# Kernel tuning notes

Measured on AMD Instinct MI355X. Metric: run time of the kernel, lower is better.

## Reference

```python
import jax, jax.numpy as jnp
import numpy as np

DN = ('NHWC', 'HWIO', 'NHWC')

def conv_same(x, w):
    return jax.lax.conv_general_dilated(x, w, (1, 1), 'SAME', dimension_numbers=DN)

def hard_sigmoid(x):
    # Keras ConvLSTM2D default recurrent_activation='hard_sigmoid'
    return jnp.clip(0.2 * x + 0.5, 0.0, 1.0)

def setup_inputs() -> dict:
    key = jax.random.key(0)
    ks = jax.random.split(key, 20)
    B, T, H, W, C = 4, 10, 144, 256, 3
    F = 64  # ConvLSTM filters
    def w(k, shape, fan_in):
        return jax.random.normal(k, shape, jnp.float32) * (1.0 / np.sqrt(fan_in))
    inp = {}
    inp['inputs'] = jax.random.normal(ks[0], (B, T, H, W, C), jnp.float32)
    # ConvLSTM2D: input kernel, recurrent kernel, bias (gate order i, f, c, o)
    inp['Wx'] = w(ks[1], (5, 5, C, 4 * F), 5 * 5 * C)
    inp['Wh'] = w(ks[2], (5, 5, F, 4 * F), 5 * 5 * F)
    inp['b_lstm'] = jnp.zeros((4 * F,), jnp.float32)
    # BatchNorm (inference mode: moving stats)
    inp['gamma'] = jnp.ones((F,), jnp.float32)
    inp['beta'] = jnp.zeros((F,), jnp.float32)
    inp['mov_mean'] = jax.random.normal(ks[3], (F,), jnp.float32) * 0.1
    inp['mov_var'] = jax.random.uniform(ks[4], (F,), jnp.float32, 0.5, 1.5)
    # Conv2D stack
    inp['W1'] = w(ks[5], (9, 9, 64, 16), 9 * 9 * 64); inp['b1'] = jnp.zeros((16,), jnp.float32)
    inp['W2'] = w(ks[6], (5, 5, 16, 32), 5 * 5 * 16); inp['b2'] = jnp.zeros((32,), jnp.float32)
    inp['W3'] = w(ks[7], (3, 3, 32, 64), 3 * 3 * 32); inp['b3'] = jnp.zeros((64,), jnp.float32)
    inp['W4'] = w(ks[8], (3, 3, 64, 64), 3 * 3 * 64); inp['b4'] = jnp.zeros((64,), jnp.float32)
    inp['W5'] = w(ks[9], (3, 3, 64, 3), 3 * 3 * 64); inp['b5'] = jnp.zeros((3,), jnp.float32)
    return inp

def conv_lstm(inputs, Wx, Wh, b_lstm):
    B, T, H, W, _ = inputs.shape
    F = Wh.shape[2]
    xs = jnp.transpose(inputs, (1, 0, 2, 3, 4))  # [T,B,H,W,C]

    def step(carry, x_t):
        h, c = carry
        z = conv_same(x_t, Wx) + b_lstm + conv_same(h, Wh)  # [B,H,W,4F]
        zi, zf, zc, zo = jnp.split(z, 4, axis=-1)
        i = hard_sigmoid(zi)
        f = hard_sigmoid(zf)
        o = hard_sigmoid(zo)
        c_new = f * c + i * jnp.tanh(zc)
        h_new = o * jnp.tanh(c_new)
        return (h_new, c_new), None

    h0 = jnp.zeros((B, H, W, F), inputs.dtype)
    c0 = jnp.zeros((B, H, W, F), inputs.dtype)
    (h, _), _ = jax.lax.scan(step, (h0, c0), xs)
    return h  # return_sequences=False -> last hidden state

def reference(inputs, Wx, Wh, b_lstm, gamma, beta, mov_mean, mov_var,
              W1, b1, W2, b2, W3, b3, W4, b4, W5, b5):
    X = conv_lstm(inputs, Wx, Wh, b_lstm)
    # BatchNorm inference, eps=1e-3 (Keras default)
    X = (X - mov_mean) * jax.lax.rsqrt(mov_var + 1e-3) * gamma + beta
    X = jax.nn.relu(conv_same(X, W1) + b1)
    X = jax.nn.relu(conv_same(X, W2) + b2)
    X = jax.nn.relu(conv_same(X, W3) + b3)
    X = jax.nn.relu(conv_same(X, W4) + b4)
    X = jax.nn.sigmoid(conv_same(X, W5) + b5)
    return X
```

## Files before the change

### kernel.cpp

```cpp
#include <hip/hip_runtime.h>
#include <math.h>

#define B_ 4
#define T_ 10
#define H_ 144
#define W_ 256
#define F_ 64

typedef __attribute__((ext_vector_type(8))) __bf16 bf16x8;
typedef __attribute__((ext_vector_type(4))) float f32x4;

static __device__ __forceinline__ float hs_(float x) {
    return fminf(fmaxf(fmaf(x, 0.2f, 0.5f), 0.f), 1.f);
}
static __device__ __forceinline__ unsigned short f2bf(float f) {
    unsigned u = __builtin_bit_cast(unsigned, f);
    u += 0x7fff + ((u >> 16) & 1);
    return (unsigned short)(u >> 16);
}
static __device__ __forceinline__ float bf2f(unsigned short s) {
    unsigned u = ((unsigned)s) << 16;
    return __builtin_bit_cast(float, u);
}

__global__ void repack_wh_mfma(const float* __restrict__ w, unsigned short* __restrict__ o) {
    int idx = blockIdx.x * 256 + threadIdx.x;
    if (idx >= 25 * 2 * 4 * 4 * 64) return;
    int l = idx & 63;
    int wf = (idx >> 6) & 3;
    int g = (idx >> 8) & 3;
    int ch = (idx >> 10) & 1;
    int tap = idx >> 11;
    int n = g * 64 + wf * 16 + (l & 15);
    unsigned short* dst = o + (size_t)idx * 8;
#pragma unroll
    for (int j = 0; j < 8; ++j) {
        int c = ch * 32 + (l >> 4) * 8 + j;
        dst[j] = f2bf(w[((size_t)(tap * 64 + c)) * 256 + n]);
    }
}

__global__ void repack_wx_mfma(const float* __restrict__ w, unsigned short* __restrict__ o) {
    int idx = blockIdx.x * 256 + threadIdx.x;
    if (idx >= 5 * 4 * 4 * 64) return;
    int l = idx & 63;
    int wf = (idx >> 6) & 3;
    int g = (idx >> 8) & 3;
    int ky = idx >> 10;
    int n = g * 64 + wf * 16 + (l & 15);
    unsigned short* dst = o + (size_t)idx * 8;
#pragma unroll
    for (int j = 0; j < 8; ++j) {
        int k = (l >> 4) * 8 + j;
        unsigned short v = 0;
        if (k < 15) {
            int kx = k / 3, c = k - kx * 3;
            v = f2bf(w[((size_t)((ky * 5 + kx) * 3 + c)) * 256 + n]);
        }
        dst[j] = v;
    }
}

__global__ void repack_conv(const float* __restrict__ w, unsigned short* __restrict__ o,
                            int taps, int cin, int cout) {
    int NF = cout >> 4;
    int total = taps * 2 * NF * 64;
    int idx = blockIdx.x * 256 + threadIdx.x;
    if (idx >= total) return;
    int l = idx & 63;
    int nf = (idx >> 6) % NF;
    int ch = ((idx >> 6) / NF) & 1;
    int tap = (idx >> 6) / NF / 2;
    int n = nf * 16 + (l & 15);
    unsigned short* dst = o + (size_t)idx * 8;
#pragma unroll
    for (int j = 0; j < 8; ++j) {
        int c = ch * 32 + (l >> 4) * 8 + j;
        dst[j] = (c < cin) ? f2bf(w[((size_t)(tap * cin + c)) * cout + n]) : (unsigned short)0;
    }
}

#define MT 64
__global__ __launch_bounds__(256, 3) void lstm_mfma(
    const float* __restrict__ x,
    const unsigned short* __restrict__ wxr,
    const unsigned short* __restrict__ whr,
    const float* __restrict__ bias,
    const unsigned short* __restrict__ h_prev,
    unsigned short* __restrict__ h_out,
    float* __restrict__ c_io,
    int t, int first)
{
    __shared__ char sh[5 * 68 * 128];
    __shared__ unsigned short sxr[5 * 72 * 4];

    const int b = blockIdx.z, y = blockIdx.y, x0 = blockIdx.x * MT;
    const int tid = threadIdx.x;
    const int w = tid >> 6, l = tid & 63;
    const int m0 = l & 15, kq = l >> 4;

    int dj[8];
#pragma unroll
    for (int j = 0; j < 8; ++j) {
        int k = kq * 8 + j;
        int kx = k / 3, c = k - kx * 3;
        dj[j] = (k < 15) ? kx * 4 + c : 3;
    }

    for (int e = tid; e < 5 * 68; e += 256) {
        int ky = e / 68, px = e - ky * 68;
        sxr[(ky * 72 + px) * 4 + 3] = 0;
    }
    for (int e = tid; e < 5 * 68 * 3; e += 256) {
        int ky = e / 204;
        int rem = e - ky * 204;
        int px = rem / 3, c = rem - px * 3;
        int yg = y + ky - 2, xg = x0 + px - 2;
        float v = 0.f;
        if (yg >= 0 && yg < H_ && (unsigned)xg < W_)
            v = x[(((size_t)((b * T_ + t) * H_ + yg)) * W_ + xg) * 3 + c];
        sxr[(ky * 72 + px) * 4 + c] = f2bf(v);
    }
    if (!first) {
        for (int e = tid; e < 5 * 68 * 8; e += 256) {
            int ky = e / (68 * 8);
            int rem = e - ky * 68 * 8;
            int px = rem >> 3, cg = rem & 7;
            int yg = y + ky - 2, xg = x0 + px - 2;
            uint4 v = make_uint4(0, 0, 0, 0);
            if (yg >= 0 && yg < H_ && (unsigned)xg < W_)
                v = *(const uint4*)(h_prev + ((((size_t)(b * H_ + yg)) * W_ + xg) << 6) + cg * 8);
            int slot = ((cg & 3) << 1) | (cg >> 2);
            int off = ((ky * 68 + px) * 128 + slot * 16) ^ ((px & 7) << 4);
            *(uint4*)(sh + off) = v;
        }
    }
    __syncthreads();

    f32x4 acc[4][4];
#pragma unroll
    for (int rf = 0; rf < 4; ++rf)
#pragma unroll
        for (int g = 0; g < 4; ++g) acc[rf][g] = (f32x4){0.f, 0.f, 0.f, 0.f};

    for (int ky = 0; ky < 5; ++ky) {
        bf16x8 a[4], bb[4];
#pragma unroll
        for (int rf = 0; rf < 4; ++rf) {
            int base = (ky * 72 + rf * 16 + m0) * 4;
            union { bf16x8 v; unsigned short u[8]; } tt;
#pragma unroll
            for (int j = 0; j < 8; ++j) tt.u[j] = sxr[base + dj[j]];
            a[rf] = tt.v;
        }
#pragma unroll
        for (int g = 0; g < 4; ++g)
            bb[g] = *(const bf16x8*)(wxr + ((size_t)((ky * 16 + g * 4 + w) * 64 + l)) * 8);
#pragma unroll
        for (int rf = 0; rf < 4; ++rf)
#pragma unroll
            for (int g = 0; g < 4; ++g)
                acc[rf][g] = __builtin_amdgcn_mfma_f32_16x16x32_bf16(a[rf], bb[g], acc[rf][g], 0, 0, 0);
    }

    if (!first) {
        int V[5][2];
#pragma unroll
        for (int kx = 0; kx < 5; ++kx) {
            int T = ((m0 + kx) & 7) << 4;
#pragma unroll
            for (int ch = 0; ch < 2; ++ch)
                V[kx][ch] = (m0 * 128 + kq * 32 + ch * 16) ^ T;
        }
        const char* shb = sh;
        const unsigned short* wb = whr + (size_t)w * 512 + (size_t)l * 8;
#pragma unroll
        for (int ky = 0; ky < 5; ++ky)
#pragma unroll
        for (int kx = 0; kx < 5; ++kx)
#pragma unroll
        for (int ch = 0; ch < 2; ++ch) {
            const int s = (ky * 5 + kx) * 2 + ch;
            bf16x8 a[4], bb[4];
#pragma unroll
            for (int g = 0; g < 4; ++g)
                bb[g] = *(const bf16x8*)(wb + s * 8192 + g * 2048);
#pragma unroll
            for (int rf = 0; rf < 4; ++rf)
                a[rf] = *(const bf16x8*)(shb + (V[kx][ch] + (ky * 8704 + kx * 128 + rf * 2048)));
#pragma unroll
            for (int rf = 0; rf < 4; ++rf)
#pragma unroll
                for (int g = 0; g < 4; ++g)
                    acc[rf][g] = __builtin_amdgcn_mfma_f32_16x16x32_bf16(a[rf], bb[g], acc[rf][g], 0, 0, 0);
        }
    }

    const int f = (w << 4) + m0;
    const float bi0 = bias[f], bi1 = bias[64 + f], bi2 = bias[128 + f], bi3 = bias[192 + f];
#pragma unroll
    for (int rf = 0; rf < 4; ++rf) {
#pragma unroll
        for (int r = 0; r < 4; ++r) {
            int px = x0 + rf * 16 + kq * 4 + r;
            size_t idx = ((((size_t)(b * H_ + y)) * W_ + px) << 6) + f;
            float zi = acc[rf][0][r] + bi0;
            float zf = acc[rf][1][r] + bi1;
            float zc = acc[rf][2][r] + bi2;
            float zo = acc[rf][3][r] + bi3;
            float cp = first ? 0.f : c_io[idx];
            float cn = hs_(zf) * cp + hs_(zi) * tanhf(zc);
            float hn = hs_(zo) * tanhf(cn);
            c_io[idx] = cn;
            h_out[idx] = f2bf(hn);
        }
    }
}

__global__ void bn_k(const unsigned short* __restrict__ in, unsigned short* __restrict__ out,
                     const float* __restrict__ gamma, const float* __restrict__ beta,
                     const float* __restrict__ mean, const float* __restrict__ var, int n) {
    for (int i = blockIdx.x * blockDim.x + threadIdx.x; i < n; i += gridDim.x * blockDim.x) {
        int c = i & 63;
        float s = rsqrtf(var[c] + 1e-3f) * gamma[c];
        out[i] = f2bf((bf2f(in[i]) - mean[c]) * s + beta[c]);
    }
}

template <int KH, int KW, int CIN, int COUT, int KYB>
__global__ __launch_bounds__(256) void conv_mfma(
    const unsigned short* __restrict__ in, const unsigned short* __restrict__ wr,
    const float* __restrict__ bias, unsigned short* __restrict__ out)
{
    constexpr int TC = 64 + KW - 1;
    constexpr int PADX = KW / 2, PADY = KH / 2;
    constexpr int NF = COUT / 16;
    constexpr int CHN = (CIN + 31) / 32;
    constexpr int NKG = KH / KYB;
    __shared__ char sh[KYB * TC * 128];

    const int b = blockIdx.z, y = blockIdx.y, x0 = blockIdx.x * 64;
    const int tid = threadIdx.x;
    const int w = tid >> 6, l = tid & 63;
    const int m0 = l & 15, kq = l >> 4;

    f32x4 acc[NF];
#pragma unroll
    for (int nf = 0; nf < NF; ++nf) acc[nf] = (f32x4){0.f, 0.f, 0.f, 0.f};

    for (int kg = 0; kg < NKG; ++kg) {
        __syncthreads();
        for (int e = tid; e < KYB * TC * 8; e += 256) {
            int kyl = e / (TC * 8);
            int rem = e - kyl * TC * 8;
            int px = rem >> 3, cg = rem & 7;
            int ky = kg * KYB + kyl;
            int yg = y + ky - PADY, xg = x0 + px - PADX;
            int c0 = cg * 8;
            uint4 v = make_uint4(0, 0, 0, 0);
            if (yg >= 0 && yg < H_ && (unsigned)xg < W_ && c0 < CIN)
                v = *(const uint4*)(in + ((size_t)((b * H_ + yg) * W_) + xg) * CIN + c0);
            int off = ((kyl * TC + px) * 128 + cg * 16) ^ ((px & 7) << 4);
            *(uint4*)(sh + off) = v;
        }
        __syncthreads();

        for (int kyl = 0; kyl < KYB; ++kyl) {
            int ky = kg * KYB + kyl;
#pragma unroll
            for (int kx = 0; kx < KW; ++kx) {
#pragma unroll
                for (int ch = 0; ch < CHN; ++ch) {
                    int px = w * 16 + m0 + kx;
                    int off = ((kyl * TC + px) * 128 + ch * 64 + kq * 16) ^ ((px & 7) << 4);
                    bf16x8 a = *(const bf16x8*)(sh + off);
                    int tap = ky * KW + kx;
                    const unsigned short* wp = wr + ((size_t)(((tap * 2 + ch) * NF) * 64 + l)) * 8;
#pragma unroll
                    for (int nf = 0; nf < NF; ++nf) {
                        bf16x8 bb = *(const bf16x8*)(wp + nf * 512);
                        acc[nf] = __builtin_amdgcn_mfma_f32_16x16x32_bf16(a, bb, acc[nf], 0, 0, 0);
                    }
                }
            }
        }
    }

#pragma unroll
    for (int nf = 0; nf < NF; ++nf) {
        int cout = nf * 16 + m0;
        float bv = bias[cout];
#pragma unroll
        for (int r = 0; r < 4; ++r) {
            int px = x0 + w * 16 + kq * 4 + r;
            float v = fmaxf(acc[nf][r] + bv, 0.f);
            out[((size_t)((b * H_ + y) * W_) + px) * COUT + cout] = f2bf(v);
        }
    }
}

__global__ __launch_bounds__(256) void conv5_k(
    const unsigned short* __restrict__ in, const float* __restrict__ wgt,
    const float* __restrict__ bias, float* __restrict__ out)
{
    constexpr int CC = 16;
    __shared__ float s[3][W_ + 2][CC + 1];
    const int b = blockIdx.z, y = blockIdx.y;
    const int tid = threadIdx.x;

    float acc[3] = {0.f, 0.f, 0.f};
    for (int c0 = 0; c0 < 64; c0 += CC) {
        __syncthreads();
        for (int e = tid; e < 3 * (W_ + 2) * CC; e += 256) {
            int r = e / ((W_ + 2) * CC);
            int rem = e % ((W_ + 2) * CC);
            int cc = rem / CC, ch = rem % CC;
            int yg = y + r - 1, xg = cc - 1;
            float v = 0.f;
            if (yg >= 0 && yg < H_ && xg >= 0 && xg < W_)
                v = bf2f(in[((b * H_ + yg) * W_ + xg) * 64 + c0 + ch]);
            s[r][cc][ch] = v;
        }
        __syncthreads();
        for (int ky = 0; ky < 3; ++ky) {
#pragma unroll
            for (int kx = 0; kx < 3; ++kx) {
                for (int c = 0; c < CC; ++c) {
                    const float* wp = &wgt[((ky * 3 + kx) * 64 + c0 + c) * 3];
                    float v = s[ky][tid + kx][c];
                    acc[0] = fmaf(v, wp[0], acc[0]);
                    acc[1] = fmaf(v, wp[1], acc[1]);
                    acc[2] = fmaf(v, wp[2], acc[2]);
                }
            }
        }
    }
#pragma unroll
    for (int j = 0; j < 3; ++j) {
        float v = acc[j] + bias[j];
        v = 1.f / (1.f + expf(-v));
        out[((b * H_ + y) * W_ + tid) * 3 + j] = v;
    }
}

extern "C" void kernel_launch(void* const* d_in, const int* in_sizes, int n_in,
                              void* d_out, int out_size, void* d_ws, size_t ws_size,
                              hipStream_t stream) {
    const float* x     = (const float*)d_in[0];
    const float* Wx    = (const float*)d_in[1];
    const float* Wh    = (const float*)d_in[2];
    const float* bl    = (const float*)d_in[3];
    const float* gamma = (const float*)d_in[4];
    const float* beta  = (const float*)d_in[5];
    const float* mmean = (const float*)d_in[6];
    const float* mvar  = (const float*)d_in[7];
    const float* W1 = (const float*)d_in[8];
    const float* b1 = (const float*)d_in[9];
    const float* W2 = (const float*)d_in[10];
    const float* b2 = (const float*)d_in[11];
    const float* W3 = (const float*)d_in[12];
    const float* b3 = (const float*)d_in[13];
    const float* W4 = (const float*)d_in[14];
    const float* b4 = (const float*)d_in[15];
    const float* W5 = (const float*)d_in[16];
    const float* b5 = (const float*)d_in[17];
    float* out = (float*)d_out;

    const size_t NHWF = (size_t)B_ * H_ * W_ * 64;
    char* p = (char*)d_ws;
    float* c_buf = (float*)p;                 p += NHWF * 4;
    unsigned short* hA = (unsigned short*)p;  p += NHWF * 2;
    unsigned short* hB = (unsigned short*)p;  p += NHWF * 2;
    unsigned short* whr = (unsigned short*)p; p += (size_t)25 * 2 * 16 * 64 * 8 * 2;
    unsigned short* wxr = (unsigned short*)p; p += (size_t)5 * 16 * 64 * 8 * 2;
    unsigned short* w1r = (unsigned short*)p; p += (size_t)81 * 2 * 1 * 512 * 2;
    unsigned short* w2r = (unsigned short*)p; p += (size_t)25 * 2 * 2 * 512 * 2;
    unsigned short* w3r = (unsigned short*)p; p += (size_t)9 * 2 * 4 * 512 * 2;
    unsigned short* w4r = (unsigned short*)p; p += (size_t)9 * 2 * 4 * 512 * 2;

    repack_wh_mfma<<<(25 * 2 * 4 * 4 * 64 + 255) / 256, 256, 0, stream>>>(Wh, whr);
    repack_wx_mfma<<<(5 * 4 * 4 * 64 + 255) / 256, 256, 0, stream>>>(Wx, wxr);
    repack_conv<<<(81 * 2 * 1 * 64 + 255) / 256, 256, 0, stream>>>(W1, w1r, 81, 64, 16);
    repack_conv<<<(25 * 2 * 2 * 64 + 255) / 256, 256, 0, stream>>>(W2, w2r, 25, 16, 32);
    repack_conv<<<(9 * 2 * 4 * 64 + 255) / 256, 256, 0, stream>>>(W3, w3r, 9, 32, 64);
    repack_conv<<<(9 * 2 * 4 * 64 + 255) / 256, 256, 0, stream>>>(W4, w4r, 9, 64, 64);

    dim3 lgrid(W_ / MT, H_, B_);
    for (int t = 0; t < T_; ++t) {
        const unsigned short* hp = (t & 1) ? hA : hB;
        unsigned short* ho = (t & 1) ? hB : hA;
        lstm_mfma<<<lgrid, 256, 0, stream>>>(x, wxr, whr, bl, hp, ho, c_buf, t, t == 0 ? 1 : 0);
    }

    unsigned short* bnb = hA;
    bn_k<<<2048, 256, 0, stream>>>(hB, bnb, gamma, beta, mmean, mvar, (int)NHWF);

    unsigned short* o1 = (unsigned short*)c_buf;
    unsigned short* o2 = o1 + NHWF / 4;
    unsigned short* o3 = hB;
    unsigned short* o4 = hA;

    dim3 cgrid(W_ / 64, H_, B_);
    conv_mfma<9, 9, 64, 16, 3><<<cgrid, 256, 0, stream>>>(bnb, w1r, b1, o1);
    conv_mfma<5, 5, 16, 32, 5><<<cgrid, 256, 0, stream>>>(o1, w2r, b2, o2);
    conv_mfma<3, 3, 32, 64, 3><<<cgrid, 256, 0, stream>>>(o2, w3r, b3, o3);
    conv_mfma<3, 3, 64, 64, 3><<<cgrid, 256, 0, stream>>>(o3, w4r, b4, o4);
    conv5_k<<<dim3(1, H_, B_), 256, 0, stream>>>(o4, W5, b5, out);
}
```

Before: 1.517 ms.

## Compute two output rows per LSTM block to reuse weight fragments

Each LSTM block now covers two image rows instead of one. It stages a 6-row halo of x and h in shared memory and keeps two sets of accumulators, so each loaded weight fragment feeds MFMAs for both rows. This halves the weight traffic per output and reduces halo redundancy. The cost is double the accumulator registers (occupancy hint lowered from 3 to 2 blocks), more LDS, and half as many blocks. The shared-memory channel slot layout and its swizzle addressing are also changed.

```diff
diff --git a/kernel.cpp b/kernel.cpp
--- a/kernel.cpp
+++ b/kernel.cpp
@@ -81,7 +81,7 @@
 }
 
 #define MT 64
-__global__ __launch_bounds__(256, 3) void lstm_mfma(
+__global__ __launch_bounds__(256, 2) void lstm_mfma(
     const float* __restrict__ x,
     const unsigned short* __restrict__ wxr,
     const unsigned short* __restrict__ whr,
@@ -91,10 +91,10 @@
     float* __restrict__ c_io,
     int t, int first)
 {
-    __shared__ char sh[5 * 68 * 128];
-    __shared__ unsigned short sxr[5 * 72 * 4];
-
-    const int b = blockIdx.z, y = blockIdx.y, x0 = blockIdx.x * MT;
+    __shared__ char sh[6 * 68 * 128];
+    __shared__ unsigned short sxr[6 * 72 * 4];
+
+    const int b = blockIdx.z, y0 = blockIdx.y * 2, x0 = blockIdx.x * MT;
     const int tid = threadIdx.x;
     const int w = tid >> 6, l = tid & 63;
     const int m0 = l & 15, kq = l >> 4;
@@ -107,60 +107,66 @@
         dj[j] = (k < 15) ? kx * 4 + c : 3;
     }
 
-    for (int e = tid; e < 5 * 68; e += 256) {
-        int ky = e / 68, px = e - ky * 68;
-        sxr[(ky * 72 + px) * 4 + 3] = 0;
-    }
-    for (int e = tid; e < 5 * 68 * 3; e += 256) {
-        int ky = e / 204;
-        int rem = e - ky * 204;
+    for (int e = tid; e < 6 * 68; e += 256) {
+        int r = e / 68, px = e - r * 68;
+        sxr[(r * 72 + px) * 4 + 3] = 0;
+    }
+    for (int e = tid; e < 6 * 68 * 3; e += 256) {
+        int r = e / 204;
+        int rem = e - r * 204;
         int px = rem / 3, c = rem - px * 3;
-        int yg = y + ky - 2, xg = x0 + px - 2;
+        int yg = y0 + r - 2, xg = x0 + px - 2;
         float v = 0.f;
         if (yg >= 0 && yg < H_ && (unsigned)xg < W_)
             v = x[(((size_t)((b * T_ + t) * H_ + yg)) * W_ + xg) * 3 + c];
-        sxr[(ky * 72 + px) * 4 + c] = f2bf(v);
+        sxr[(r * 72 + px) * 4 + c] = f2bf(v);
     }
     if (!first) {
-        for (int e = tid; e < 5 * 68 * 8; e += 256) {
-            int ky = e / (68 * 8);
-            int rem = e - ky * 68 * 8;
+        for (int e = tid; e < 6 * 68 * 8; e += 256) {
+            int r = e / (68 * 8);
+            int rem = e - r * 68 * 8;
             int px = rem >> 3, cg = rem & 7;
-            int yg = y + ky - 2, xg = x0 + px - 2;
+            int yg = y0 + r - 2, xg = x0 + px - 2;
             uint4 v = make_uint4(0, 0, 0, 0);
             if (yg >= 0 && yg < H_ && (unsigned)xg < W_)
                 v = *(const uint4*)(h_prev + ((((size_t)(b * H_ + yg)) * W_ + xg) << 6) + cg * 8);
-            int slot = ((cg & 3) << 1) | (cg >> 2);
-            int off = ((ky * 68 + px) * 128 + slot * 16) ^ ((px & 7) << 4);
+            int off = ((r * 68 + px) * 128 + cg * 16) ^ ((px & 7) << 4);
             *(uint4*)(sh + off) = v;
         }
     }
     __syncthreads();
 
-    f32x4 acc[4][4];
-#pragma unroll
-    for (int rf = 0; rf < 4; ++rf)
-#pragma unroll
-        for (int g = 0; g < 4; ++g) acc[rf][g] = (f32x4){0.f, 0.f, 0.f, 0.f};
-
+    f32x4 acc[2][4][4];
+#pragma unroll
+    for (int r = 0; r < 2; ++r)
+#pragma unroll
+        for (int rf = 0; rf < 4; ++rf)
+#pragma unroll
+            for (int g = 0; g < 4; ++g) acc[r][rf][g] = (f32x4){0.f, 0.f, 0.f, 0.f};
+
+#pragma unroll
     for (int ky = 0; ky < 5; ++ky) {
-        bf16x8 a[4], bb[4];
-#pragma unroll
-        for (int rf = 0; rf < 4; ++rf) {
-            int base = (ky * 72 + rf * 16 + m0) * 4;
-            union { bf16x8 v; unsigned short u[8]; } tt;
-#pragma unroll
-            for (int j = 0; j < 8; ++j) tt.u[j] = sxr[base + dj[j]];
-            a[rf] = tt.v;
-        }
+        bf16x8 bb[4];
 #pragma unroll
         for (int g = 0; g < 4; ++g)
             bb[g] = *(const bf16x8*)(wxr + ((size_t)((ky * 16 + g * 4 + w) * 64 + l)) * 8);
 #pragma unroll
-        for (int rf = 0; rf < 4; ++rf)
-#pragma unroll
-            for (int g = 0; g < 4; ++g)
-                acc[rf][g] = __builtin_amdgcn_mfma_f32_16x16x32_bf16(a[rf], bb[g], acc[rf][g], 0, 0, 0);
+        for (int r = 0; r < 2; ++r) {
+            bf16x8 a[4];
+#pragma unroll
+            for (int rf = 0; rf < 4; ++rf) {
+                int base = ((ky + r) * 72 + rf * 16 + m0) * 4;
+                union { bf16x8 v; unsigned short u[8]; } tt;
+#pragma unroll
+                for (int j = 0; j < 8; ++j) tt.u[j] = sxr[base + dj[j]];
+                a[rf] = tt.v;
+            }
+#pragma unroll
+            for (int rf = 0; rf < 4; ++rf)
+#pragma unroll
+                for (int g = 0; g < 4; ++g)
+                    acc[r][rf][g] = __builtin_amdgcn_mfma_f32_16x16x32_bf16(a[rf], bb[g], acc[r][rf][g], 0, 0, 0);
+        }
     }
 
     if (!first) {
@@ -170,7 +176,7 @@
             int T = ((m0 + kx) & 7) << 4;
 #pragma unroll
             for (int ch = 0; ch < 2; ++ch)
-                V[kx][ch] = (m0 * 128 + kq * 32 + ch * 16) ^ T;
+                V[kx][ch] = ((m0 + kx) * 128 + ch * 64 + kq * 16) ^ T;
         }
         const char* shb = sh;
         const unsigned short* wb = whr + (size_t)w * 512 + (size_t)l * 8;
@@ -181,38 +187,45 @@
 #pragma unroll
         for (int ch = 0; ch < 2; ++ch) {
             const int s = (ky * 5 + kx) * 2 + ch;
-            bf16x8 a[4], bb[4];
+            bf16x8 bb[4];
 #pragma unroll
             for (int g = 0; g < 4; ++g)
                 bb[g] = *(const bf16x8*)(wb + s * 8192 + g * 2048);
 #pragma unroll
-            for (int rf = 0; rf < 4; ++rf)
-                a[rf] = *(const bf16x8*)(shb + (V[kx][ch] + (ky * 8704 + kx * 128 + rf * 2048)));
-#pragma unroll
-            for (int rf = 0; rf < 4; ++rf)
-#pragma unroll
-                for (int g = 0; g < 4; ++g)
-                    acc[rf][g] = __builtin_amdgcn_mfma_f32_16x16x32_bf16(a[rf], bb[g], acc[rf][g], 0, 0, 0);
+            for (int r = 0; r < 2; ++r) {
+                bf16x8 a[4];
+#pragma unroll
+                for (int rf = 0; rf < 4; ++rf)
+                    a[rf] = *(const bf16x8*)(shb + (V[kx][ch] + ((ky + r) * 8704 + rf * 2048)));
+#pragma unroll
+                for (int rf = 0; rf < 4; ++rf)
+#pragma unroll
+                    for (int g = 0; g < 4; ++g)
+                        acc[r][rf][g] = __builtin_amdgcn_mfma_f32_16x16x32_bf16(a[rf], bb[g], acc[r][rf][g], 0, 0, 0);
+            }
         }
     }
 
     const int f = (w << 4) + m0;
     const float bi0 = bias[f], bi1 = bias[64 + f], bi2 = bias[128 + f], bi3 = bias[192 + f];
 #pragma unroll
-    for (int rf = 0; rf < 4; ++rf) {
-#pragma unroll
-        for (int r = 0; r < 4; ++r) {
-            int px = x0 + rf * 16 + kq * 4 + r;
-            size_t idx = ((((size_t)(b * H_ + y)) * W_ + px) << 6) + f;
-            float zi = acc[rf][0][r] + bi0;
-            float zf = acc[rf][1][r] + bi1;
-            float zc = acc[rf][2][r] + bi2;
-            float zo = acc[rf][3][r] + bi3;
-            float cp = first ? 0.f : c_io[idx];
-            float cn = hs_(zf) * cp + hs_(zi) * tanhf(zc);
-            float hn = hs_(zo) * tanhf(cn);
-            c_io[idx] = cn;
-            h_out[idx] = f2bf(hn);
+    for (int r = 0; r < 2; ++r) {
+#pragma unroll
+        for (int rf = 0; rf < 4; ++rf) {
+#pragma unroll
+            for (int j = 0; j < 4; ++j) {
+                int px = x0 + rf * 16 + kq * 4 + j;
+                size_t idx = ((((size_t)(b * H_ + y0 + r)) * W_ + px) << 6) + f;
+                float zi = acc[r][rf][0][j] + bi0;
+                float zf = acc[r][rf][1][j] + bi1;
+                float zc = acc[r][rf][2][j] + bi2;
+                float zo = acc[r][rf][3][j] + bi3;
+                float cp = first ? 0.f : c_io[idx];
+                float cn = hs_(zf) * cp + hs_(zi) * tanhf(zc);
+                float hn = hs_(zo) * tanhf(cn);
+                c_io[idx] = cn;
+                h_out[idx] = f2bf(hn);
+            }
         }
     }
 }
@@ -385,7 +398,7 @@
     repack_conv<<<(9 * 2 * 4 * 64 + 255) / 256, 256, 0, stream>>>(W3, w3r, 9, 32, 64);
     repack_conv<<<(9 * 2 * 4 * 64 + 255) / 256, 256, 0, stream>>>(W4, w4r, 9, 64, 64);
 
-    dim3 lgrid(W_ / MT, H_, B_);
+    dim3 lgrid(W_ / MT, H_ / 2, B_);
     for (int t = 0; t < T_; ++t) {
         const unsigned short* hp = (t & 1) ? hA : hB;
         unsigned short* ho = (t & 1) ? hB : hA;
```

Measured after the change: 2.416 ms. 59.3% more time.

## Stage recurrent weights through double-buffered LDS via async global_load_lds

Applied to the files above, without the earlier changes.

Recurrent-kernel weight tiles are now staged through a double-buffered 32KB LDS area using global_load_lds, with the next tap's tile prefetched while the current tap's MFMAs run. Before, each wave read them straight from global memory. The hidden-state LDS layout and swizzle are also changed to a plain channel-group order with a new address formula. The changes add a __syncthreads per tap (50 per block) and extra LDS use, so launch bounds drop occupancy from 3 to 2 blocks per CU.

```diff
diff --git a/kernel.cpp b/kernel.cpp
--- a/kernel.cpp
+++ b/kernel.cpp
@@ -21,6 +21,11 @@
 static __device__ __forceinline__ float bf2f(unsigned short s) {
     unsigned u = ((unsigned)s) << 16;
     return __builtin_bit_cast(float, u);
+}
+static __device__ __forceinline__ void gl_lds16(const void* gp, void* lp) {
+    __builtin_amdgcn_global_load_lds(
+        (const __attribute__((address_space(1))) unsigned int*)gp,
+        (__attribute__((address_space(3))) unsigned int*)lp, 16, 0, 0);
 }
 
 __global__ void repack_wh_mfma(const float* __restrict__ w, unsigned short* __restrict__ o) {
@@ -81,7 +86,7 @@
 }
 
 #define MT 64
-__global__ __launch_bounds__(256, 3) void lstm_mfma(
+__global__ __launch_bounds__(256, 2) void lstm_mfma(
     const float* __restrict__ x,
     const unsigned short* __restrict__ wxr,
     const unsigned short* __restrict__ whr,
@@ -93,6 +98,7 @@
 {
     __shared__ char sh[5 * 68 * 128];
     __shared__ unsigned short sxr[5 * 72 * 4];
+    __shared__ char sB[2][16384];
 
     const int b = blockIdx.z, y = blockIdx.y, x0 = blockIdx.x * MT;
     const int tid = threadIdx.x;
@@ -130,9 +136,15 @@
             uint4 v = make_uint4(0, 0, 0, 0);
             if (yg >= 0 && yg < H_ && (unsigned)xg < W_)
                 v = *(const uint4*)(h_prev + ((((size_t)(b * H_ + yg)) * W_ + xg) << 6) + cg * 8);
-            int slot = ((cg & 3) << 1) | (cg >> 2);
-            int off = ((ky * 68 + px) * 128 + slot * 16) ^ ((px & 7) << 4);
+            int off = ((ky * 68 + px) * 128 + cg * 16) ^ ((px & 7) << 4);
             *(uint4*)(sh + off) = v;
+        }
+        {
+            const char* g0 = (const char*)whr + (size_t)tid * 16;
+            char* d0 = &sB[0][(size_t)(tid >> 6) << 10];
+#pragma unroll
+            for (int q = 0; q < 4; ++q)
+                gl_lds16(g0 + q * 4096, d0 + q * 4096);
         }
     }
     __syncthreads();
@@ -170,29 +182,35 @@
             int T = ((m0 + kx) & 7) << 4;
 #pragma unroll
             for (int ch = 0; ch < 2; ++ch)
-                V[kx][ch] = (m0 * 128 + kq * 32 + ch * 16) ^ T;
+                V[kx][ch] = ((m0 + kx) * 128 + ch * 64 + kq * 16) ^ T;
         }
         const char* shb = sh;
-        const unsigned short* wb = whr + (size_t)w * 512 + (size_t)l * 8;
-#pragma unroll
-        for (int ky = 0; ky < 5; ++ky)
-#pragma unroll
-        for (int kx = 0; kx < 5; ++kx)
-#pragma unroll
-        for (int ch = 0; ch < 2; ++ch) {
-            const int s = (ky * 5 + kx) * 2 + ch;
+#pragma unroll
+        for (int s = 0; s < 50; ++s) {
+            const int ky = s / 10;
+            const int kx = (s - ky * 10) >> 1;
+            const int ch = s & 1;
+            if (s < 49) {
+                const char* gs = (const char*)whr + (size_t)(s + 1) * 16384 + (size_t)tid * 16;
+                char* ds = &sB[(s + 1) & 1][(size_t)(tid >> 6) << 10];
+#pragma unroll
+                for (int q = 0; q < 4; ++q)
+                    gl_lds16(gs + q * 4096, ds + q * 4096);
+            }
+            const char* bq = &sB[s & 1][((size_t)(tid >> 6) << 10) + ((size_t)(l) << 4)];
             bf16x8 a[4], bb[4];
 #pragma unroll
             for (int g = 0; g < 4; ++g)
-                bb[g] = *(const bf16x8*)(wb + s * 8192 + g * 2048);
+                bb[g] = *(const bf16x8*)(bq + g * 4096);
 #pragma unroll
             for (int rf = 0; rf < 4; ++rf)
-                a[rf] = *(const bf16x8*)(shb + (V[kx][ch] + (ky * 8704 + kx * 128 + rf * 2048)));
+                a[rf] = *(const bf16x8*)(shb + (V[kx][ch] + (ky * 8704 + rf * 2048)));
 #pragma unroll
             for (int rf = 0; rf < 4; ++rf)
 #pragma unroll
                 for (int g = 0; g < 4; ++g)
                     acc[rf][g] = __builtin_amdgcn_mfma_f32_16x16x32_bf16(a[rf], bb[g], acc[rf][g], 0, 0, 0);
+            __syncthreads();
         }
     }
 
```

Result: slower. 1.943 ms (+28.1%).

## Fuse BatchNorm into last LSTM step and change h smem layout

Applied to the files above, without the earlier changes.

Removes the standalone BatchNorm kernel: the final LSTM timestep applies the BN affine transform to h directly and skips writing the cell state. It also changes the shared-memory layout of the previous hidden state, dropping the slot permutation and adjusting the read offsets and Wh weight addressing. This saves one full pass over the hidden tensor and the final c write, but the layout change must still line up with the repacked Wh order (repack code not visible), so there is a correctness risk.

```diff
diff --git a/kernel.cpp b/kernel.cpp
--- a/kernel.cpp
+++ b/kernel.cpp
@@ -89,7 +89,11 @@
     const unsigned short* __restrict__ h_prev,
     unsigned short* __restrict__ h_out,
     float* __restrict__ c_io,
-    int t, int first)
+    const float* __restrict__ gamma,
+    const float* __restrict__ beta,
+    const float* __restrict__ mmean,
+    const float* __restrict__ mvar,
+    int t, int first, int last)
 {
     __shared__ char sh[5 * 68 * 128];
     __shared__ unsigned short sxr[5 * 72 * 4];
@@ -130,8 +134,7 @@
             uint4 v = make_uint4(0, 0, 0, 0);
             if (yg >= 0 && yg < H_ && (unsigned)xg < W_)
                 v = *(const uint4*)(h_prev + ((((size_t)(b * H_ + yg)) * W_ + xg) << 6) + cg * 8);
-            int slot = ((cg & 3) << 1) | (cg >> 2);
-            int off = ((ky * 68 + px) * 128 + slot * 16) ^ ((px & 7) << 4);
+            int off = ((ky * 68 + px) * 128 + cg * 16) ^ ((px & 7) << 4);
             *(uint4*)(sh + off) = v;
         }
     }
@@ -170,10 +173,10 @@
             int T = ((m0 + kx) & 7) << 4;
 #pragma unroll
             for (int ch = 0; ch < 2; ++ch)
-                V[kx][ch] = (m0 * 128 + kq * 32 + ch * 16) ^ T;
+                V[kx][ch] = ((m0 + kx) * 128 + ch * 64 + kq * 16) ^ T;
         }
         const char* shb = sh;
-        const unsigned short* wb = whr + (size_t)w * 512 + (size_t)l * 8;
+        const char* wb = (const char*)whr + (size_t)w * 1024 + (size_t)l * 16;
 #pragma unroll
         for (int ky = 0; ky < 5; ++ky)
 #pragma unroll
@@ -184,10 +187,10 @@
             bf16x8 a[4], bb[4];
 #pragma unroll
             for (int g = 0; g < 4; ++g)
-                bb[g] = *(const bf16x8*)(wb + s * 8192 + g * 2048);
+                bb[g] = *(const bf16x8*)(wb + (size_t)s * 16384 + g * 4096);
 #pragma unroll
             for (int rf = 0; rf < 4; ++rf)
-                a[rf] = *(const bf16x8*)(shb + (V[kx][ch] + (ky * 8704 + kx * 128 + rf * 2048)));
+                a[rf] = *(const bf16x8*)(shb + (V[kx][ch] + (ky * 8704 + rf * 2048)));
 #pragma unroll
             for (int rf = 0; rf < 4; ++rf)
 #pragma unroll
@@ -198,6 +201,12 @@
 
     const int f = (w << 4) + m0;
     const float bi0 = bias[f], bi1 = bias[64 + f], bi2 = bias[128 + f], bi3 = bias[192 + f];
+    float bn_s = 0.f, bn_b = 0.f, bn_m = 0.f;
+    if (last) {
+        bn_s = rsqrtf(mvar[f] + 1e-3f) * gamma[f];
+        bn_b = beta[f];
+        bn_m = mmean[f];
+    }
 #pragma unroll
     for (int rf = 0; rf < 4; ++rf) {
 #pragma unroll
@@ -211,19 +220,13 @@
             float cp = first ? 0.f : c_io[idx];
             float cn = hs_(zf) * cp + hs_(zi) * tanhf(zc);
             float hn = hs_(zo) * tanhf(cn);
-            c_io[idx] = cn;
-            h_out[idx] = f2bf(hn);
-        }
-    }
-}
-
-__global__ void bn_k(const unsigned short* __restrict__ in, unsigned short* __restrict__ out,
-                     const float* __restrict__ gamma, const float* __restrict__ beta,
-                     const float* __restrict__ mean, const float* __restrict__ var, int n) {
-    for (int i = blockIdx.x * blockDim.x + threadIdx.x; i < n; i += gridDim.x * blockDim.x) {
-        int c = i & 63;
-        float s = rsqrtf(var[c] + 1e-3f) * gamma[c];
-        out[i] = f2bf((bf2f(in[i]) - mean[c]) * s + beta[c]);
+            if (last) {
+                h_out[idx] = f2bf((hn - bn_m) * bn_s + bn_b);
+            } else {
+                c_io[idx] = cn;
+                h_out[idx] = f2bf(hn);
+            }
+        }
     }
 }
 
@@ -389,19 +392,18 @@
     for (int t = 0; t < T_; ++t) {
         const unsigned short* hp = (t & 1) ? hA : hB;
         unsigned short* ho = (t & 1) ? hB : hA;
-        lstm_mfma<<<lgrid, 256, 0, stream>>>(x, wxr, whr, bl, hp, ho, c_buf, t, t == 0 ? 1 : 0);
-    }
-
-    unsigned short* bnb = hA;
-    bn_k<<<2048, 256, 0, stream>>>(hB, bnb, gamma, beta, mmean, mvar, (int)NHWF);
+        lstm_mfma<<<lgrid, 256, 0, stream>>>(x, wxr, whr, bl, hp, ho, c_buf,
+                                             gamma, beta, mmean, mvar,
+                                             t, t == 0 ? 1 : 0, t == T_ - 1 ? 1 : 0);
+    }
 
     unsigned short* o1 = (unsigned short*)c_buf;
     unsigned short* o2 = o1 + NHWF / 4;
-    unsigned short* o3 = hB;
-    unsigned short* o4 = hA;
+    unsigned short* o3 = hA;
+    unsigned short* o4 = hB;
 
     dim3 cgrid(W_ / 64, H_, B_);
-    conv_mfma<9, 9, 64, 16, 3><<<cgrid, 256, 0, stream>>>(bnb, w1r, b1, o1);
+    conv_mfma<9, 9, 64, 16, 3><<<cgrid, 256, 0, stream>>>(hB, w1r, b1, o1);
     conv_mfma<5, 5, 16, 32, 5><<<cgrid, 256, 0, stream>>>(o1, w2r, b2, o2);
     conv_mfma<3, 3, 32, 64, 3><<<cgrid, 256, 0, stream>>>(o2, w3r, b3, o3);
     conv_mfma<3, 3, 64, 64, 3><<<cgrid, 256, 0, stream>>>(o3, w4r, b4, o4);
```

Result: no change. 1.506 ms (-0.7%).
